# Optimization experiments

Measured on AMD Instinct MI355X. Metric: run time of the kernel, lower is better.

The kernel has to match this reference:

```python
import jax, jax.numpy as jnp
import numpy as np

EPS = 1e-5  # nn.LayerNorm default
TOP_K = 2


def setup_inputs() -> dict:
    key = jax.random.key(0)
    ks = jax.random.split(key, 8)
    B, S, D, H, E = 4, 2048, 512, 512, 8
    sd = lambda fan_in: 1.0 / np.sqrt(fan_in)
    x = jax.random.normal(ks[0], (B, S, D), dtype=jnp.float32)
    # gate: Linear(D, E, bias=False)
    Wg = jax.random.uniform(ks[1], (D, E), jnp.float32, -sd(D), sd(D))
    # stacked expert params (ExpertModule): fc1 D->H, fc2 H->D, LayerNorm(D)
    W1 = jax.random.uniform(ks[2], (E, D, H), jnp.float32, -sd(D), sd(D))
    b1 = jax.random.uniform(ks[3], (E, H), jnp.float32, -sd(D), sd(D))
    W2 = jax.random.uniform(ks[4], (E, H, D), jnp.float32, -sd(H), sd(H))
    b2 = jax.random.uniform(ks[5], (E, D), jnp.float32, -sd(H), sd(H))
    gamma = jnp.ones((E, D), jnp.float32)
    beta = jnp.zeros((E, D), jnp.float32)
    return {"x": x, "Wg": Wg, "W1": W1, "b1": b1, "W2": W2, "b2": b2,
            "gamma": gamma, "beta": beta}


def _moe_forward(x, Wg, W1, b1, W2, b2, gamma, beta):
    B, S, D = x.shape
    xf = x.reshape(-1, D)                                   # [T, D]
    # gating: top-k logits then softmax over the k selected logits only
    logits = xf @ Wg                                        # [T, E]
    topv, topi = jax.lax.top_k(logits, TOP_K)               # [T, K]
    gate_w = jax.nn.softmax(topv, axis=-1)                  # [T, K]
    # expert MLP + LayerNorm computed for all experts (dropout inactive in eval)
    h = jax.nn.relu(jnp.einsum('td,edh->teh', xf, W1) + b1[None])   # [T, E, H]
    y = jnp.einsum('teh,ehd->ted', h, W2) + b2[None]                 # [T, E, D]
    mu = jnp.mean(y, axis=-1, keepdims=True)
    var = jnp.mean((y - mu) ** 2, axis=-1, keepdims=True)
    y = (y - mu) / jnp.sqrt(var + EPS) * gamma[None] + beta[None]
    # combine: gather the k selected expert outputs and weight-sum
    y_sel = jnp.take_along_axis(y, topi[:, :, None], axis=1)        # [T, K, D]
    out = jnp.sum(gate_w[:, :, None] * y_sel, axis=1)               # [T, D]
    return out.reshape(B, S, D)


def reference(x, Wg, W1, b1, W2, b2, gamma, beta):
    return _moe_forward(x, Wg, W1, b1, W2, b2, gamma, beta)
```

## Files before the change

kernel.cpp:

```cpp
#include <hip/hip_runtime.h>
#include <hip/hip_bf16.h>


#define T_TOK   8192
#define DDIM    512
#define HDIM    512
#define NEXP    8
#define NASSIGN (T_TOK * 2)
#define CPAD    16
#define CAP     4096
#define MT      20

typedef _Float16 f16x8 __attribute__((ext_vector_type(8)));
typedef _Float16 f16x4 __attribute__((ext_vector_type(4)));
typedef float    f32x4 __attribute__((ext_vector_type(4)));

__device__ __forceinline__ void gld_lds16(const _Float16* g, _Float16* l) {
    __builtin_amdgcn_global_load_lds(
        (const __attribute__((address_space(1))) unsigned int*)g,
        (__attribute__((address_space(3))) unsigned int*)l,
        16, 0, 0);
}

__global__ __launch_bounds__(1024) void prep_kernel(
    const float* __restrict__ x,
    const float* __restrict__ Wg,
    const float* __restrict__ W1,
    const float* __restrict__ W2,
    _Float16* __restrict__ xh,
    int* __restrict__ ei,
    float* __restrict__ gw,
    int* __restrict__ cursor,
    int* __restrict__ rowtok,
    int* __restrict__ pos,
    _Float16* __restrict__ W1t,
    _Float16* __restrict__ W2t)
{
    __shared__ float smf[4 * 32 * 33];
    __shared__ int earr[32];

    int bid = blockIdx.x;
    int tid = threadIdx.x;

    if (bid < 512) {
        float (*wgt)[512] = (float (*)[512])smf;
        int lane = tid & 63;
        int wave = tid >> 6;
        int t = bid * 16 + wave;

        const float* xr = x + (size_t)t * DDIM;
        float4 xv0 = *(const float4*)(xr + lane * 4);
        float4 xv1 = *(const float4*)(xr + 256 + lane * 4);

        if (tid < 256) {
#pragma unroll
            for (int r = 0; r < 2; r++) {
                int d = r * 256 + tid;
                const float4* wr = (const float4*)(Wg + (size_t)d * NEXP);
                float4 a = wr[0], b = wr[1];
                wgt[0][d] = a.x; wgt[1][d] = a.y; wgt[2][d] = a.z; wgt[3][d] = a.w;
                wgt[4][d] = b.x; wgt[5][d] = b.y; wgt[6][d] = b.z; wgt[7][d] = b.w;
            }
        }

        {
            f16x4 h0, h1;
            h0[0] = (_Float16)xv0.x; h0[1] = (_Float16)xv0.y;
            h0[2] = (_Float16)xv0.z; h0[3] = (_Float16)xv0.w;
            h1[0] = (_Float16)xv1.x; h1[1] = (_Float16)xv1.y;
            h1[2] = (_Float16)xv1.z; h1[3] = (_Float16)xv1.w;
            *(f16x4*)(xh + (size_t)t * DDIM + lane * 4) = h0;
            *(f16x4*)(xh + (size_t)t * DDIM + 256 + lane * 4) = h1;
        }
        __syncthreads();

        double acc[NEXP];
#pragma unroll
        for (int e = 0; e < NEXP; e++) acc[e] = 0.0;
#pragma unroll
        for (int jj = 0; jj < 2; jj++) {
            float4 xv = jj ? xv1 : xv0;
            int d0 = jj * 256 + lane * 4;
            double xd[4] = {(double)xv.x, (double)xv.y, (double)xv.z, (double)xv.w};
#pragma unroll
            for (int e = 0; e < NEXP; e++) {
                f32x4 wv = *(const f32x4*)(&wgt[e][d0]);
#pragma unroll
                for (int c = 0; c < 4; c++)
                    acc[e] += xd[c] * (double)wv[c];
            }
        }
#pragma unroll
        for (int off = 1; off < 8; off <<= 1) {
#pragma unroll
            for (int e = 0; e < NEXP; e++) acc[e] += __shfl_xor(acc[e], off, 64);
        }
        double v = acc[0];
#pragma unroll
        for (int e = 1; e < NEXP; e++) if ((lane & 7) == e) v = acc[e];
#pragma unroll
        for (int off = 8; off < 64; off <<= 1) v += __shfl_xor(v, off, 64);
        double lv[NEXP];
#pragma unroll
        for (int e = 0; e < NEXP; e++) lv[e] = __shfl(v, e, 64);

        double v0 = -1e300; int i0 = 0;
#pragma unroll
        for (int e = 0; e < NEXP; e++) if (lv[e] > v0) { v0 = lv[e]; i0 = e; }
        double v1 = -1e300; int i1 = (i0 == 0) ? 1 : 0;
#pragma unroll
        for (int e = 0; e < NEXP; e++) if (e != i0 && lv[e] > v1) { v1 = lv[e]; i1 = e; }

        if (lane == 0) {
            double ex = exp(v1 - v0);
            float g0 = (float)(1.0 / (1.0 + ex));
            float g1 = (float)(ex / (1.0 + ex));
            ei[2 * t] = i0;  ei[2 * t + 1] = i1;
            gw[2 * t] = g0;  gw[2 * t + 1] = g1;
            earr[wave * 2] = i0;
            earr[wave * 2 + 1] = i1;
        }
        __syncthreads();

        if (wave == 0) {
            int e = (lane < 32) ? earr[lane] : -1;
            int r = 0;
#pragma unroll
            for (int ex = 0; ex < NEXP; ex++) {
                unsigned long long mask = __ballot(e == ex);
                if (e == ex) {
                    int leader = __ffsll(mask) - 1;
                    int cnt = __popcll(mask);
                    unsigned long long below = mask & ((1ull << lane) - 1ull);
                    int base = 0;
                    if (lane == leader) base = atomicAdd(&cursor[ex * CPAD], cnt);
                    base = __shfl(base, leader, 64);
                    r = ex * CAP + base + __popcll(below);
                }
            }
            if (lane < 32) {
                int s = bid * 32 + lane;
                rowtok[r] = s;
                pos[s] = r;
            }
        }
    } else {
        float (*tile)[32][33] = (float (*)[32][33])smf;
        int sub = tid >> 8;
        int stid = tid & 255;
        int b2 = (bid - 512) * 4 + sub;
        int z = b2 >> 8;
        int rem = b2 & 255;
        int by = (rem >> 4) * 32;
        int bx = (rem & 15) * 32;
        const float* src;
        _Float16* dst;
        if (z < 8) { src = W1 + (size_t)z * 512 * 512; dst = W1t + (size_t)z * 512 * 512; }
        else       { src = W2 + (size_t)(z - 8) * 512 * 512; dst = W2t + (size_t)(z - 8) * 512 * 512; }
        int tx = stid & 31, ty = stid >> 5;
#pragma unroll
        for (int i = 0; i < 4; i++) {
            int r = by + ty + i * 8;
            tile[sub][ty + i * 8][tx] = src[(size_t)r * 512 + bx + tx];
        }
        __syncthreads();
        int row = stid >> 3;
        int jc  = stid & 7;
        f16x4 v;
#pragma unroll
        for (int k = 0; k < 4; k++) v[k] = (_Float16)tile[sub][jc * 4 + k][row];
        *(f16x4*)(dst + (size_t)(bx + row) * 512 + by + jc * 4) = v;
    }
}

template <bool GATHER, bool RELU>
__global__ __launch_bounds__(256) void gemm_tile(
    const _Float16* __restrict__ A,
    const _Float16* __restrict__ Bt,
    const float* __restrict__ bias,
    const int* __restrict__ rowtok,
    const int* __restrict__ cursor,
    _Float16* __restrict__ C)
{
    int bid = blockIdx.x;
    int e = bid & 7;
    int j = bid >> 3;
    int ne = cursor[e * CPAD];
    int m0 = (j >> 2) * 128;
    if (m0 >= ne) return;
    int n0 = (j & 3) * 128;
    int off = e * CAP;
    const _Float16* Bte = Bt + (size_t)e * 512 * 512;

    __shared__ _Float16 As[2][128 * 32];
    __shared__ _Float16 Bs[2][128 * 32];

    int tid = threadIdx.x;
    int lane = tid & 63;
    int wave = tid >> 6;
    int wm = (wave >> 1) * 64;
    int wn = (wave & 1) * 64;
    int quad = lane >> 4;
    int l16 = lane & 15;

    int srow = tid >> 2;
    int ksw = ((tid & 3) ^ ((srow >> 1) & 3)) * 8;

    int r0g = m0 + srow;
    int r1g = m0 + srow + 64;
    int cr0 = off + (r0g < ne ? r0g : ne - 1);
    int cr1 = off + (r1g < ne ? r1g : ne - 1);
    const _Float16* arow0;
    const _Float16* arow1;
    if (GATHER) {
        arow0 = A + (size_t)(rowtok[cr0] >> 1) * 512;
        arow1 = A + (size_t)(rowtok[cr1] >> 1) * 512;
    } else {
        arow0 = A + (size_t)cr0 * 512;
        arow1 = A + (size_t)cr1 * 512;
    }
    const _Float16* brow0 = Bte + (size_t)(n0 + srow) * 512;
    const _Float16* brow1 = Bte + (size_t)(n0 + srow + 64) * 512;

    f32x4 acc[4][4];
#pragma unroll
    for (int i = 0; i < 4; i++)
#pragma unroll
        for (int jj = 0; jj < 4; jj++) {
            acc[i][jj][0] = 0.f; acc[i][jj][1] = 0.f;
            acc[i][jj][2] = 0.f; acc[i][jj][3] = 0.f;
        }

    int rsw = (quad ^ ((l16 >> 1) & 3)) * 8;

    gld_lds16(arow0 + ksw, &As[0][tid * 8]);
    gld_lds16(arow1 + ksw, &As[0][tid * 8 + 64 * 32]);
    gld_lds16(brow0 + ksw, &Bs[0][tid * 8]);
    gld_lds16(brow1 + ksw, &Bs[0][tid * 8 + 64 * 32]);
    __syncthreads();

    int cur = 0;
    for (int t = 0; t < 16; ++t) {
        if (t < 15) {
            int k1 = (t + 1) * 32;
            gld_lds16(arow0 + k1 + ksw, &As[cur ^ 1][tid * 8]);
            gld_lds16(arow1 + k1 + ksw, &As[cur ^ 1][tid * 8 + 64 * 32]);
            gld_lds16(brow0 + k1 + ksw, &Bs[cur ^ 1][tid * 8]);
            gld_lds16(brow1 + k1 + ksw, &Bs[cur ^ 1][tid * 8 + 64 * 32]);
        }

        f16x8 af[4], bf[4];
#pragma unroll
        for (int i = 0; i < 4; i++)
            af[i] = *(const f16x8*)(&As[cur][(wm + i * 16 + l16) * 32 + rsw]);
#pragma unroll
        for (int jj = 0; jj < 4; jj++)
            bf[jj] = *(const f16x8*)(&Bs[cur][(wn + jj * 16 + l16) * 32 + rsw]);
#pragma unroll
        for (int i = 0; i < 4; i++)
#pragma unroll
            for (int jj = 0; jj < 4; jj++)
                acc[i][jj] = __builtin_amdgcn_mfma_f32_16x16x32_f16(af[i], bf[jj], acc[i][jj], 0, 0, 0);

        if (t < 15) {
            __syncthreads();
            cur ^= 1;
        }
    }

    float bcol[4];
#pragma unroll
    for (int jj = 0; jj < 4; jj++) bcol[jj] = bias[(size_t)e * 512 + n0 + wn + jj * 16 + l16];
#pragma unroll
    for (int i = 0; i < 4; i++) {
#pragma unroll
        for (int rr = 0; rr < 4; rr++) {
            int rg = m0 + wm + i * 16 + quad * 4 + rr;
            if (rg < ne) {
#pragma unroll
                for (int jj = 0; jj < 4; jj++) {
                    float v = acc[i][jj][rr] + bcol[jj];
                    if (RELU) v = fmaxf(v, 0.0f);
                    C[(size_t)(off + rg) * 512 + n0 + wn + jj * 16 + l16] = (_Float16)v;
                }
            }
        }
    }
}

__global__ void ln_combine_kernel(const _Float16* __restrict__ yb,
                                  const int* __restrict__ pos,
                                  const float* __restrict__ gw,
                                  const int* __restrict__ ei,
                                  const float* __restrict__ gamma,
                                  const float* __restrict__ beta,
                                  float* __restrict__ out) {
    int t = blockIdx.x * 4 + (threadIdx.x >> 6);
    int lane = threadIdx.x & 63;
    float o[8];
#pragma unroll
    for (int j = 0; j < 8; j++) o[j] = 0.0f;

    int2 pr = *(const int2*)(pos + 2 * t);
    int2 er = *(const int2*)(ei + 2 * t);
    float2 gr = *(const float2*)(gw + 2 * t);

#pragma unroll
    for (int k = 0; k < 2; k++) {
        int r = k ? pr.y : pr.x;
        int e = k ? er.y : er.x;
        float w = k ? gr.y : gr.x;
        f16x8 v = *(const f16x8*)(yb + (size_t)r * 512 + lane * 8);
        const float4* gp = (const float4*)(gamma + (size_t)e * 512 + lane * 8);
        const float4* bp = (const float4*)(beta + (size_t)e * 512 + lane * 8);
        float4 ga = gp[0], gb = gp[1];
        float4 ba = bp[0], bb = bp[1];
        float gvv[8] = {ga.x, ga.y, ga.z, ga.w, gb.x, gb.y, gb.z, gb.w};
        float bvv[8] = {ba.x, ba.y, ba.z, ba.w, bb.x, bb.y, bb.z, bb.w};
        float f[8];
        float sum = 0.f, sq = 0.f;
#pragma unroll
        for (int j = 0; j < 8; j++) { f[j] = (float)v[j]; sum += f[j]; sq += f[j] * f[j]; }
#pragma unroll
        for (int off = 1; off < 64; off <<= 1) {
            sum += __shfl_xor(sum, off, 64);
            sq  += __shfl_xor(sq, off, 64);
        }
        float mu = sum * (1.0f / 512.0f);
        float var = sq * (1.0f / 512.0f) - mu * mu;
        float rstd = rsqrtf(var + 1e-5f);
#pragma unroll
        for (int j = 0; j < 8; j++)
            o[j] += w * ((f[j] - mu) * rstd * gvv[j] + bvv[j]);
    }
    float4* op = (float4*)(out + (size_t)t * 512 + lane * 8);
    op[0] = make_float4(o[0], o[1], o[2], o[3]);
    op[1] = make_float4(o[4], o[5], o[6], o[7]);
}

extern "C" void kernel_launch(void* const* d_in, const int* in_sizes, int n_in,
                              void* d_out, int out_size, void* d_ws, size_t ws_size,
                              hipStream_t stream) {
    const float* x     = (const float*)d_in[0];
    const float* Wg    = (const float*)d_in[1];
    const float* W1    = (const float*)d_in[2];
    const float* b1    = (const float*)d_in[3];
    const float* W2    = (const float*)d_in[4];
    const float* b2    = (const float*)d_in[5];
    const float* gamma = (const float*)d_in[6];
    const float* beta  = (const float*)d_in[7];
    float* out = (float*)d_out;

    char* w = (char*)d_ws;
    size_t o = 0;
    auto alloc = [&](size_t bytes) -> void* {
        void* p = w + o;
        o += (bytes + 255) & ~(size_t)255;
        return p;
    };
    _Float16* xh  = (_Float16*)alloc((size_t)T_TOK * DDIM * 2);
    _Float16* W1t = (_Float16*)alloc((size_t)NEXP * DDIM * HDIM * 2);
    _Float16* W2t = (_Float16*)alloc((size_t)NEXP * DDIM * HDIM * 2);
    _Float16* hb  = (_Float16*)alloc((size_t)NEXP * CAP * HDIM * 2);
    _Float16* yb  = (_Float16*)alloc((size_t)NEXP * CAP * DDIM * 2);
    float* gw     = (float*)alloc((size_t)NASSIGN * 4);
    int* ei       = (int*)alloc((size_t)NASSIGN * 4);
    int* rowtok   = (int*)alloc((size_t)NEXP * CAP * 4);
    int* pos      = (int*)alloc((size_t)NASSIGN * 4);
    int* cursor   = (int*)alloc(NEXP * CPAD * 4);
    (void)ws_size; (void)n_in; (void)in_sizes; (void)out_size;

    hipMemsetAsync(cursor, 0, NEXP * CPAD * sizeof(int), stream);

    prep_kernel<<<1536, 1024, 0, stream>>>(x, Wg, W1, W2, xh, ei, gw,
                                           cursor, rowtok, pos, W1t, W2t);

    gemm_tile<true, true><<<640, 256, 0, stream>>>(xh, W1t, b1, rowtok, cursor, hb);
    gemm_tile<false, false><<<640, 256, 0, stream>>>(hb, W2t, b2, nullptr, cursor, yb);

    ln_combine_kernel<<<2048, 256, 0, stream>>>(yb, pos, gw, ei, gamma, beta, out);
}
```

Baseline: 149.3 us.

## Load GEMM A-operand fragments directly from global into registers, bypassing LDS

The A tile is no longer staged through shared memory. Each wave loads its own A fragments straight from global memory into registers, one k-step ahead, using per-row base pointers (gathered rows when gathering). This cuts LDS traffic and shared-memory footprint, which may raise occupancy. In exchange, A rows are reloaded redundantly by the two waves sharing the same rows, global accesses are 16-byte pieces per lane that are less coalesced, and register pressure goes up.

```diff
diff --git a/kernel.cpp b/kernel.cpp
--- a/kernel.cpp
+++ b/kernel.cpp
@@ -192,7 +192,6 @@
     int off = e * CAP;
     const _Float16* Bte = Bt + (size_t)e * 512 * 512;
 
-    __shared__ _Float16 As[2][128 * 32];
     __shared__ _Float16 Bs[2][128 * 32];
 
     int tid = threadIdx.x;
@@ -203,22 +202,17 @@
     int quad = lane >> 4;
     int l16 = lane & 15;
 
+    const _Float16* abase[4];
+#pragma unroll
+    for (int i = 0; i < 4; i++) {
+        int rg = m0 + wm + i * 16 + l16;
+        int cr = off + (rg < ne ? rg : ne - 1);
+        if (GATHER) abase[i] = A + (size_t)(rowtok[cr] >> 1) * 512;
+        else        abase[i] = A + (size_t)cr * 512;
+    }
+
     int srow = tid >> 2;
     int ksw = ((tid & 3) ^ ((srow >> 1) & 3)) * 8;
-
-    int r0g = m0 + srow;
-    int r1g = m0 + srow + 64;
-    int cr0 = off + (r0g < ne ? r0g : ne - 1);
-    int cr1 = off + (r1g < ne ? r1g : ne - 1);
-    const _Float16* arow0;
-    const _Float16* arow1;
-    if (GATHER) {
-        arow0 = A + (size_t)(rowtok[cr0] >> 1) * 512;
-        arow1 = A + (size_t)(rowtok[cr1] >> 1) * 512;
-    } else {
-        arow0 = A + (size_t)cr0 * 512;
-        arow1 = A + (size_t)cr1 * 512;
-    }
     const _Float16* brow0 = Bte + (size_t)(n0 + srow) * 512;
     const _Float16* brow1 = Bte + (size_t)(n0 + srow + 64) * 512;
 
@@ -233,26 +227,26 @@
 
     int rsw = (quad ^ ((l16 >> 1) & 3)) * 8;
 
-    gld_lds16(arow0 + ksw, &As[0][tid * 8]);
-    gld_lds16(arow1 + ksw, &As[0][tid * 8 + 64 * 32]);
     gld_lds16(brow0 + ksw, &Bs[0][tid * 8]);
     gld_lds16(brow1 + ksw, &Bs[0][tid * 8 + 64 * 32]);
+    f16x8 afc[4], afn[4];
+#pragma unroll
+    for (int i = 0; i < 4; i++)
+        afc[i] = *(const f16x8*)(abase[i] + quad * 8);
     __syncthreads();
 
     int cur = 0;
     for (int t = 0; t < 16; ++t) {
         if (t < 15) {
             int k1 = (t + 1) * 32;
-            gld_lds16(arow0 + k1 + ksw, &As[cur ^ 1][tid * 8]);
-            gld_lds16(arow1 + k1 + ksw, &As[cur ^ 1][tid * 8 + 64 * 32]);
             gld_lds16(brow0 + k1 + ksw, &Bs[cur ^ 1][tid * 8]);
             gld_lds16(brow1 + k1 + ksw, &Bs[cur ^ 1][tid * 8 + 64 * 32]);
-        }
-
-        f16x8 af[4], bf[4];
-#pragma unroll
-        for (int i = 0; i < 4; i++)
-            af[i] = *(const f16x8*)(&As[cur][(wm + i * 16 + l16) * 32 + rsw]);
+#pragma unroll
+            for (int i = 0; i < 4; i++)
+                afn[i] = *(const f16x8*)(abase[i] + k1 + quad * 8);
+        }
+
+        f16x8 bf[4];
 #pragma unroll
         for (int jj = 0; jj < 4; jj++)
             bf[jj] = *(const f16x8*)(&Bs[cur][(wn + jj * 16 + l16) * 32 + rsw]);
@@ -260,11 +254,13 @@
         for (int i = 0; i < 4; i++)
 #pragma unroll
             for (int jj = 0; jj < 4; jj++)
-                acc[i][jj] = __builtin_amdgcn_mfma_f32_16x16x32_f16(af[i], bf[jj], acc[i][jj], 0, 0, 0);
+                acc[i][jj] = __builtin_amdgcn_mfma_f32_16x16x32_f16(afc[i], bf[jj], acc[i][jj], 0, 0, 0);
 
         if (t < 15) {
             __syncthreads();
             cur ^= 1;
+#pragma unroll
+            for (int i = 0; i < 4; i++) afc[i] = afn[i];
         }
     }
 
```

After: 169.6 us. +13.6%, slower.
